# Kernel optimization log

Hardware: AMD Instinct MI355X
Metric: run time of the kernel (lower is better)

Reference implementation:

```python
import jax, jax.numpy as jnp
import numpy as np
from jax import lax

IN_DIM, MID_DIM, OUT_DIM, SIZE_EMBED_DIM = 1024, 512, 50, 64
N_POS = 30
B, N = 4, 512
H = MID_DIM // 2  # per-direction LSTM hidden


def _span_size_ids(n):
    ar = jnp.arange(n)
    ids = ar[None, :] - ar[:, None]          # [i,j] = j - i
    ids = jnp.where(ids < -(N_POS // 2), -(N_POS // 2), ids)
    ids = jnp.where(ids >= N_POS // 2, N_POS // 2 - 1, ids) + N_POS // 2
    return ids.astype(jnp.int32)             # values in [0, 29]


def _lstm_dir(x, Wih, Whh, bih, bhh, reverse):
    # x: (B, N, in_dim) -> (B, N, H)
    b = x.shape[0]
    xs = jnp.swapaxes(x, 0, 1)               # (N, B, in)
    init = (jnp.zeros((b, H), x.dtype), jnp.zeros((b, H), x.dtype))

    def step(carry, xt):
        h, c = carry
        g = xt @ Wih.T + h @ Whh.T + (bih + bhh)
        i, f, gg, o = jnp.split(g, 4, axis=-1)
        c = jax.nn.sigmoid(f) * c + jax.nn.sigmoid(i) * jnp.tanh(gg)
        h = jax.nn.sigmoid(o) * jnp.tanh(c)
        return (h, c), h

    _, hs = lax.scan(step, init, xs, reverse=reverse)
    return jnp.swapaxes(hs, 0, 1)


def setup_inputs() -> dict:
    key = jax.random.key(0)
    ks = jax.random.split(key, 16)
    s = 0.02
    d = {
        'input_embeds': jax.random.normal(ks[0], (B, N, IN_DIM), jnp.float32),
        'Wih_f': jax.random.normal(ks[1], (4 * H, IN_DIM)) * s,
        'Whh_f': jax.random.normal(ks[2], (4 * H, H)) * s,
        'bih_f': jnp.zeros((4 * H,)),
        'bhh_f': jnp.zeros((4 * H,)),
        'Wih_b': jax.random.normal(ks[3], (4 * H, IN_DIM)) * s,
        'Whh_b': jax.random.normal(ks[4], (4 * H, H)) * s,
        'bih_b': jnp.zeros((4 * H,)),
        'bhh_b': jnp.zeros((4 * H,)),
        'W_head': jax.random.normal(ks[5], (MID_DIM, MID_DIM)) * s,
        'b_head': jnp.zeros((MID_DIM,)),
        'W_tail': jax.random.normal(ks[6], (MID_DIM, MID_DIM)) * s,
        'b_tail': jnp.zeros((MID_DIM,)),
        'emb_table': jax.random.normal(ks[7], (N_POS, SIZE_EMBED_DIM)) * s,
        'W': jax.random.normal(ks[8], (OUT_DIM, 2 * MID_DIM + SIZE_EMBED_DIM + 2)) * s,
    }
    return d


def reference(input_embeds, Wih_f, Whh_f, bih_f, bhh_f, Wih_b, Whh_b, bih_b, bhh_b,
              W_head, b_head, W_tail, b_tail, emb_table, W):
    n = input_embeds.shape[1]
    # BiLSTM (dropouts are identity at eval)
    h_f = _lstm_dir(input_embeds, Wih_f, Whh_f, bih_f, bhh_f, reverse=False)
    h_b = _lstm_dir(input_embeds, Wih_b, Whh_b, bih_b, bhh_b, reverse=True)
    x = jnp.concatenate([h_f, h_b], axis=-1)              # (B, N, mid)
    head = jax.nn.leaky_relu(x @ W_head.T + b_head)        # (B, N, mid)
    tail = jax.nn.leaky_relu(x @ W_tail.T + b_tail)
    ones = jnp.ones_like(head[..., :1])
    head1 = jnp.concatenate([head, ones], axis=-1)         # (B, N, mid+1)
    tail1 = jnp.concatenate([tail, ones], axis=-1)
    se = emb_table[_span_size_ids(n)]                      # (N, N, se)
    # einsum('bmnh,kh->bkmn', cat([head1_m, tail1_n, se_mn]), W) decomposed:
    mp1 = MID_DIM + 1
    Wh, Wt, Ws = W[:, :mp1], W[:, mp1:2 * mp1], W[:, 2 * mp1:]
    s_head = jnp.einsum('bmh,kh->bkm', head1, Wh)          # (B, k, N)
    s_tail = jnp.einsum('bnh,kh->bkn', tail1, Wt)
    s_size = jnp.einsum('mnh,kh->kmn', se, Ws)             # (k, N, N)
    return s_head[:, :, :, None] + s_tail[:, :, None, :] + s_size[None]
```

## Files before the change

kernel.cpp:

```cpp
#include <hip/hip_runtime.h>
#include <hip/hip_bf16.h>
#include <stdint.h>


typedef float  floatx4 __attribute__((ext_vector_type(4)));
typedef short  short4v __attribute__((ext_vector_type(4)));
typedef short  short8  __attribute__((ext_vector_type(8)));
typedef int    int4v   __attribute__((ext_vector_type(4)));

#define LOG2E_F  1.4426950408889634f
#define TWOLOG2E_F 2.8853900817779268f

__device__ __forceinline__ short f2bf(float f) {
    __hip_bfloat16 h = __float2bfloat16(f);
    return *reinterpret_cast<short*>(&h);
}
__device__ __forceinline__ float fexp2(float x) {
#if __has_builtin(__builtin_amdgcn_exp2f)
    return __builtin_amdgcn_exp2f(x);
#else
    float r; asm("v_exp_f32 %0, %1" : "=v"(r) : "v"(x)); return r;
#endif
}
__device__ __forceinline__ float frcp(float x) {
#if __has_builtin(__builtin_amdgcn_rcpf)
    return __builtin_amdgcn_rcpf(x);
#else
    float r; asm("v_rcp_f32 %0, %1" : "=v"(r) : "v"(x)); return r;
#endif
}
__device__ __forceinline__ int q8i(float x) {
    int q = (int)rintf(x);
    return q > 127 ? 127 : (q < -127 ? -127 : q);
}

__global__ __launch_bounds__(256) void prep_k(
    const float* __restrict__ input_embeds,
    const float* __restrict__ Wih_f, const float* __restrict__ Wih_b,
    const float* __restrict__ W_head, const float* __restrict__ W_tail,
    const float* __restrict__ W, const float* __restrict__ emb,
    const float* __restrict__ bih_f, const float* __restrict__ bhh_f,
    const float* __restrict__ bih_b, const float* __restrict__ bhh_b,
    const float* __restrict__ b_head, const float* __restrict__ b_tail,
    float* __restrict__ ssize, float* __restrict__ sbias,
    float* __restrict__ biasc1, float* __restrict__ biasc2,
    __hip_bfloat16* __restrict__ abf, __hip_bfloat16* __restrict__ wihbf,
    __hip_bfloat16* __restrict__ wc2bf, __hip_bfloat16* __restrict__ wcbf)
{
    const int g0 = blockIdx.x * 256 + threadIdx.x;
    const int gs = gridDim.x * 256;

    for (int i4 = g0; i4 < (2048 * 1024) / 4; i4 += gs) {
        floatx4 v = *(const floatx4*)(input_embeds + (size_t)i4 * 4);
        short4v s = { f2bf(v[0]), f2bf(v[1]), f2bf(v[2]), f2bf(v[3]) };
        *(short4v*)(abf + (size_t)i4 * 4) = s;
    }
    for (int i4 = g0; i4 < (2048 * 1024) / 4; i4 += gs) {
        int r = i4 >> 8, c4 = (i4 & 255) * 4;
        const float* src = (r < 1024) ? (Wih_f + (size_t)r * 1024 + c4)
                                      : (Wih_b + (size_t)(r - 1024) * 1024 + c4);
        floatx4 v = *(const floatx4*)src;
        short4v s = { f2bf(v[0]), f2bf(v[1]), f2bf(v[2]), f2bf(v[3]) };
        *(short4v*)(wihbf + (size_t)i4 * 4) = s;
    }
    for (int i4 = g0; i4 < (1024 * 512) / 4; i4 += gs) {
        int r = i4 >> 7, c4 = (i4 & 127) * 4;
        const float* src = (r < 512) ? (W_head + (size_t)r * 512 + c4)
                                     : (W_tail + (size_t)(r - 512) * 512 + c4);
        floatx4 v = *(const floatx4*)src;
        short4v s = { f2bf(v[0]), f2bf(v[1]), f2bf(v[2]), f2bf(v[3]) };
        *(short4v*)(wc2bf + (size_t)i4 * 4) = s;
    }
    for (int i4 = g0; i4 < (128 * 512) / 4; i4 += gs) {
        int r = i4 >> 7, c4 = (i4 & 127) * 4;
        short4v s = {0, 0, 0, 0};
        if (r < 50) {
            const float* p = W + (size_t)r * 1090 + c4;
            s[0] = f2bf(p[0]); s[1] = f2bf(p[1]); s[2] = f2bf(p[2]); s[3] = f2bf(p[3]);
        } else if (r >= 64 && r < 114) {
            const float* p = W + (size_t)(r - 64) * 1090 + 513 + c4;
            s[0] = f2bf(p[0]); s[1] = f2bf(p[1]); s[2] = f2bf(p[2]); s[3] = f2bf(p[3]);
        }
        *(short4v*)(wcbf + (size_t)i4 * 4) = s;
    }

    for (int i = g0; i < 1600; i += gs) {
        int k = i >> 5, pp = i & 31;
        float acc = 0.0f;
        if (pp < 30)
            for (int h = 0; h < 64; ++h)
                acc += W[(size_t)k * 1090 + 1026 + h] * emb[pp * 64 + h];
        ssize[i] = acc;
    }
    for (int i = g0; i < 128; i += gs) {
        float v = 0.0f;
        if (i < 50)                    v = W[(size_t)i * 1090 + 512];
        else if (i >= 64 && i < 114)   v = W[(size_t)(i - 64) * 1090 + 1025];
        sbias[i] = v;
    }
    for (int i = g0; i < 2048; i += gs)
        biasc1[i] = (i < 1024) ? (bih_f[i] + bhh_f[i]) : (bih_b[i - 1024] + bhh_b[i - 1024]);
    for (int i = g0; i < 1024; i += gs)
        biasc2[i] = (i < 512) ? b_head[i] : b_tail[i - 512];
}

__global__ __launch_bounds__(256) void gemm_bt(
    const __hip_bfloat16* __restrict__ Abf, int lda,
    int a_split_n, int a_split_off,
    const __hip_bfloat16* __restrict__ Bbf, int ldb,
    const float* __restrict__ bias, int K, int mode,
    float* __restrict__ out0, __hip_bfloat16* __restrict__ out1)
{
    __shared__ __align__(16) short As[128][48];
    __shared__ __align__(16) short Bs[64][48];
    const int tid   = threadIdx.x;
    const int nbase = blockIdx.x * 64;
    const int mbase = blockIdx.y * 128;
    const int aoff  = (nbase >= a_split_n) ? a_split_off : 0;
    const int arow = tid >> 1, akq = (tid & 1) * 16;
    const int brow = tid >> 2, bkq = (tid & 3) * 8;
    const int wv = tid >> 6, ln = tid & 63, l15 = ln & 15, quad = ln >> 4;

    floatx4 acc[2][4];
#pragma unroll
    for (int i = 0; i < 2; ++i)
#pragma unroll
        for (int j = 0; j < 4; ++j) acc[i][j] = (floatx4){0.f, 0.f, 0.f, 0.f};

    const unsigned short* A = (const unsigned short*)Abf;
    const unsigned short* B = (const unsigned short*)Bbf;
    const int KI = K >> 5;
    for (int kk = 0; kk < KI; ++kk) {
        const unsigned short* pa = A + (size_t)(mbase + arow) * lda + aoff + kk * 32 + akq;
        short8 sa0 = *(const short8*)pa;
        short8 sa1 = *(const short8*)(pa + 8);
        const unsigned short* pb = B + (size_t)(nbase + brow) * ldb + kk * 32 + bkq;
        short8 sb = *(const short8*)pb;

        __syncthreads();
        *(short8*)&As[arow][akq]     = sa0;
        *(short8*)&As[arow][akq + 8] = sa1;
        *(short8*)&Bs[brow][bkq]     = sb;
        __syncthreads();

        short8 a0 = *(const short8*)&As[wv * 32 + l15][quad * 8];
        short8 a1 = *(const short8*)&As[wv * 32 + 16 + l15][quad * 8];
#pragma unroll
        for (int nt = 0; nt < 4; ++nt) {
            short8 bb = *(const short8*)&Bs[nt * 16 + l15][quad * 8];
            acc[0][nt] = __builtin_amdgcn_mfma_f32_16x16x32_bf16(a0, bb, acc[0][nt], 0, 0, 0);
            acc[1][nt] = __builtin_amdgcn_mfma_f32_16x16x32_bf16(a1, bb, acc[1][nt], 0, 0, 0);
        }
    }

#pragma unroll
    for (int mt = 0; mt < 2; ++mt)
#pragma unroll
        for (int nt = 0; nt < 4; ++nt) {
            const int gc = nbase + nt * 16 + l15;
            const float bv = bias[gc];
#pragma unroll
            for (int r = 0; r < 4; ++r) {
                const int gr = mbase + wv * 32 + mt * 16 + quad * 4 + r;
                float v = acc[mt][nt][r] + bv;
                if (mode == 0) {
                    const int d = gc >> 10, nn = gc & 1023;
                    const int gate = nn >> 8;
                    const int vrow = ((nn & 255) << 2) | gate;
                    const int t = gr & 511, b = gr >> 9;
                    const float gsc = (gate == 2) ? TWOLOG2E_F : -LOG2E_F;
                    out0[(((size_t)d * 512 + t) * 4 + b) * 1024 + vrow] = v * gsc;
                } else if (mode == 1) {
                    v = v < 0.0f ? 0.01f * v : v;
                    out1[(size_t)gr * 1024 + gc] = __float2bfloat16(v);
                } else {
                    out0[(size_t)gr * 128 + gc] = v;
                }
            }
        }
}

__global__ __launch_bounds__(1024) void lstm_k(
    const float* __restrict__ Whh_f, const float* __restrict__ Whh_b,
    const float* __restrict__ xg, __hip_bfloat16* __restrict__ hcat)
{
    const int dir = blockIdx.x;
    const float* Whh = dir ? Whh_b : Whh_f;
    const float* xgd = xg + (size_t)dir * 512 * 4 * 1024;
    __shared__ __align__(16) float sm_lds[1024];
    __shared__ __align__(16) signed char hq[2][4][64][16];
    __shared__ __align__(16) int gexch[16][64][4];
    const int tid = threadIdx.x;
    const int wv = tid >> 6, ln = tid & 63, l15 = ln & 15, quad = ln >> 4;

    for (int v = wv * 64; v < wv * 64 + 64; ++v) {
        const int orig = ((v & 3) << 8) | (v >> 2);
        floatx4 x = *(const floatx4*)(Whh + (size_t)orig * 256 + ln * 4);
        float m = fmaxf(fmaxf(fabsf(x[0]), fabsf(x[1])), fmaxf(fabsf(x[2]), fabsf(x[3])));
#pragma unroll
        for (int off = 32; off; off >>= 1) m = fmaxf(m, __shfl_xor(m, off, 64));
        if (ln == 0) sm_lds[v] = m;
    }
    for (int i = tid; i < 2 * 4 * 64 * 16 / 4; i += 1024) ((int*)hq)[i] = 0;
    __syncthreads();

    int4v afrag[4][4];
#pragma unroll
    for (int tt = 0; tt < 4; ++tt) {
        const int vrow = (wv * 4 + tt) * 16 + l15;
        const int orig = ((vrow & 3) << 8) | (vrow >> 2);
        const float sm = sm_lds[vrow];
        const float inv = sm > 1e-30f ? 127.0f / sm : 0.0f;
#pragma unroll
        for (int kf = 0; kf < 4; ++kf) {
            const float* p = Whh + (size_t)orig * 256 + kf * 64 + quad * 16;
            int4v fr;
#pragma unroll
            for (int j = 0; j < 4; ++j) {
                floatx4 w4 = *(const floatx4*)(p + j * 4);
                int b0 = q8i(w4[0] * inv), b1 = q8i(w4[1] * inv);
                int b2 = q8i(w4[2] * inv), b3 = q8i(w4[3] * inv);
                fr[j] = (b0 & 255) | ((b1 & 255) << 8) | ((b2 & 255) << 16) | (b3 << 24);
            }
            afrag[tt][kf] = fr;
        }
    }

    const int u_mine = wv * 16 + (ln >> 2);
    const int batch  = ln & 3;
    floatx4 scl;
    {
        const float sc = 1.0f / 16129.0f;
        floatx4 s4 = *(const floatx4*)&sm_lds[u_mine * 4];
        scl[0] = s4[0] * (sc * -LOG2E_F);
        scl[1] = s4[1] * (sc * -LOG2E_F);
        scl[2] = s4[2] * (sc *  TWOLOG2E_F);
        scl[3] = s4[3] * (sc * -LOG2E_F);
    }
    signed char* hq_w = &hq[0][u_mine >> 6][(((u_mine >> 4) & 3) << 4) + batch][u_mine & 15];
    const int t0 = dir ? 511 : 0;
    const ptrdiff_t xstep = dir ? -4096 : 4096;
    const ptrdiff_t hstep = dir ? -512 : 512;
    const float* xp = xgd + (size_t)batch * 1024 + u_mine * 4 + (size_t)t0 * 4096;
    __hip_bfloat16* hc_p = hcat + (size_t)batch * 512 * 512 + dir * 256 + u_mine
                                + (size_t)t0 * 512;

    float c = 0.0f;
    const int4v z4 = {0, 0, 0, 0};
    __syncthreads();

    floatx4 xga = *(const floatx4*)xp;
    floatx4 xgb;

#define LSTM_STEP(P, XC, XN)                                                    \
    {                                                                           \
        xp += xstep;                                                            \
        XN = *(const floatx4*)xp;   \
        int4v bb0 = *(const int4v*)&hq[P][0][ln][0];                            \
        int4v bb1 = *(const int4v*)&hq[P][1][ln][0];                            \
        int4v bb2 = *(const int4v*)&hq[P][2][ln][0];                            \
        int4v bb3 = *(const int4v*)&hq[P][3][ln][0];                            \
        int4v acc[4];                                                           \
        _Pragma("unroll")                                                       \
        for (int tt = 0; tt < 4; ++tt) {                                        \
            int4v t0v = __builtin_amdgcn_mfma_i32_16x16x64_i8(                  \
                afrag[tt][0], bb0, z4, 0, 0, 0);                                \
            t0v = __builtin_amdgcn_mfma_i32_16x16x64_i8(                        \
                afrag[tt][1], bb1, t0v, 0, 0, 0);                               \
            t0v = __builtin_amdgcn_mfma_i32_16x16x64_i8(                        \
                afrag[tt][2], bb2, t0v, 0, 0, 0);                               \
            acc[tt] = __builtin_amdgcn_mfma_i32_16x16x64_i8(                    \
                afrag[tt][3], bb3, t0v, 0, 0, 0);                               \
        }                                                                       \
        if (l15 < 4) {                                                          \
            _Pragma("unroll")                                                   \
            for (int tt = 0; tt < 4; ++tt)                                      \
                *(int4v*)&gexch[wv][(tt * 4 + quad) * 4 + l15][0] = acc[tt];    \
        }                                                                       \
        int4v g = *(const int4v*)&gexch[wv][ln][0];                             \
        float gi = fmaf((float)g[0], scl[0], XC[0]);                            \
        float gf = fmaf((float)g[1], scl[1], XC[1]);                            \
        float gg = fmaf((float)g[2], scl[2], XC[2]);                            \
        float go = fmaf((float)g[3], scl[3], XC[3]);                            \
        float iv = frcp(1.0f + fexp2(gi));           \
        float fv = frcp(1.0f + fexp2(gf));                                      \
        float tg = fmaf(-2.0f, frcp(1.0f + fexp2(gg)), 1.0f);         \
        float ov = frcp(1.0f + fexp2(go));                                      \
        c = fmaf(fv, c, iv * tg);                                               \
        float tc = fmaf(-2.0f, frcp(1.0f + fexp2(c * TWOLOG2E_F)), 1.0f);       \
        float h = ov * tc;                                                      \
        *hc_p = __float2bfloat16(h);                                            \
        hq_w[(P) ? 0 : 4096] = (signed char)(int)rintf(h * 127.0f);  \
        hc_p += hstep;                                                          \
        asm volatile("s_waitcnt lgkmcnt(0)" ::: "memory");                      \
        __builtin_amdgcn_s_barrier();                                           \
        __builtin_amdgcn_sched_barrier(0);                                      \
        asm volatile("" ::: "memory");                                          \
    }

    for (int s = 0; s < 512; s += 2) {
        LSTM_STEP(0, xga, xgb)
        LSTM_STEP(1, xgb, xga)
    }
#undef LSTM_STEP
}

__global__ __launch_bounds__(256) void final_k(
    const float* __restrict__ sarr, const float* __restrict__ ssize,
    float* __restrict__ out)
{
    const int mb = blockIdx.x * 64;
    const int k  = blockIdx.y;
    const int b  = blockIdx.z;
    __shared__ float st[512];
    __shared__ float sh[64];
    __shared__ float ss[32];
    const int tid = threadIdx.x;
    for (int n = tid; n < 512; n += 256)
        st[n] = sarr[((size_t)b * 512 + n) * 128 + 64 + k];
    if (tid < 64) sh[tid] = sarr[((size_t)b * 512 + mb + tid) * 128 + k];
    if (tid < 32) ss[tid] = ssize[k * 32 + tid];
    __syncthreads();
    const int n4 = (tid & 127) * 4;
    const int m0 = tid >> 7;
    float* ob = out + (((size_t)b * 50 + k) * 512 + mb) * 512;
    for (int mi = m0; mi < 64; mi += 2) {
        const int m = mb + mi;
        const float base = sh[mi];
        floatx4 v;
#pragma unroll
        for (int e = 0; e < 4; ++e) {
            int d = n4 + e - m;
            d = d < -15 ? -15 : (d > 14 ? 14 : d);
            v[e] = base + st[n4 + e] + ss[d + 15];
        }
        *(floatx4*)(ob + (size_t)mi * 512 + n4) = v;
    }
}

extern "C" void kernel_launch(void* const* d_in, const int* in_sizes, int n_in,
                              void* d_out, int out_size, void* d_ws, size_t ws_size,
                              hipStream_t stream)
{
    const float* input_embeds = (const float*)d_in[0];
    const float* Wih_f  = (const float*)d_in[1];
    const float* Whh_f  = (const float*)d_in[2];
    const float* bih_f  = (const float*)d_in[3];
    const float* bhh_f  = (const float*)d_in[4];
    const float* Wih_b  = (const float*)d_in[5];
    const float* Whh_b  = (const float*)d_in[6];
    const float* bih_b  = (const float*)d_in[7];
    const float* bhh_b  = (const float*)d_in[8];
    const float* W_head = (const float*)d_in[9];
    const float* b_head = (const float*)d_in[10];
    const float* W_tail = (const float*)d_in[11];
    const float* b_tail = (const float*)d_in[12];
    const float* emb    = (const float*)d_in[13];
    const float* W      = (const float*)d_in[14];
    float* out = (float*)d_out;

    char* w = (char*)d_ws;
    float* xg     = (float*)w;  w += (size_t)2 * 512 * 4 * 1024 * 4;
    float* biasc1 = (float*)w;  w += 2048 * 4;
    float* biasc2 = (float*)w;  w += 1024 * 4;
    float* sbias  = (float*)w;  w += 128 * 4;
    float* ssize  = (float*)w;  w += 1600 * 4;
    __hip_bfloat16* wcbf  = (__hip_bfloat16*)w;  w += (size_t)128 * 512 * 2;
    __hip_bfloat16* wihbf = (__hip_bfloat16*)w;  w += (size_t)2048 * 1024 * 2;
    __hip_bfloat16* hcat  = (__hip_bfloat16*)w;  w += (size_t)2048 * 512 * 2;
    float* sarr = (float*)w;
    __hip_bfloat16* wc2bf = (__hip_bfloat16*)w;  w += (size_t)1024 * 512 * 2;
    __hip_bfloat16* abf   = (__hip_bfloat16*)w;
    __hip_bfloat16* ht    = (__hip_bfloat16*)w;  w += (size_t)2048 * 1024 * 2;

    hipLaunchKernelGGL(prep_k, dim3(64), dim3(256), 0, stream,
        input_embeds, Wih_f, Wih_b, W_head, W_tail, W, emb,
        bih_f, bhh_f, bih_b, bhh_b, b_head, b_tail,
        ssize, sbias, biasc1, biasc2, abf, wihbf, wc2bf, wcbf);

    hipLaunchKernelGGL(gemm_bt, dim3(32, 16), dim3(256), 0, stream,
        abf, 1024, 1 << 30, 0,
        wihbf, 1024, biasc1, 1024, 0, xg, (__hip_bfloat16*)nullptr);

    hipLaunchKernelGGL(lstm_k, dim3(2), dim3(1024), 0, stream, Whh_f, Whh_b, xg, hcat);

    hipLaunchKernelGGL(gemm_bt, dim3(16, 16), dim3(256), 0, stream,
        hcat, 512, 1 << 30, 0,
        wc2bf, 512, biasc2, 512, 1, (float*)nullptr, ht);

    hipLaunchKernelGGL(gemm_bt, dim3(2, 16), dim3(256), 0, stream,
        ht, 1024, 64, 512,
        wcbf, 512, sbias, 512, 2, sarr, (__hip_bfloat16*)nullptr);

    hipLaunchKernelGGL(final_k, dim3(8, 50, 4), dim3(256), 0, stream, sarr, ssize, out);
}
```

Baseline: 859.9 us.

## Compact LSTM h buffer, reorder gate layout, transpose score array, nontemporal output stores

Several layout changes land together. The input-gate GEMM now writes the gate projections gate-major, and each LSTM thread gathers its four gates with strided scalar loads. The quantized hidden-state LDS buffer is shrunk to only the batch columns that are actually used, with lanes outside them feeding zero B-fragments. The head/tail score array is stored transposed so the final kernel reads it contiguously, and the final kernel's large output is written with nontemporal stores to avoid polluting the cache. The risk is that four scalar loads per step replace one vector load on the serial recurrence path.

```diff
diff --git a/kernel.cpp b/kernel.cpp
--- a/kernel.cpp
+++ b/kernel.cpp
@@ -165,16 +165,15 @@
                 float v = acc[mt][nt][r] + bv;
                 if (mode == 0) {
                     const int d = gc >> 10, nn = gc & 1023;
-                    const int gate = nn >> 8;
-                    const int vrow = ((nn & 255) << 2) | gate;
+                    const int g = nn >> 8, u = nn & 255;
                     const int t = gr & 511, b = gr >> 9;
-                    const float gsc = (gate == 2) ? TWOLOG2E_F : -LOG2E_F;
-                    out0[(((size_t)d * 512 + t) * 4 + b) * 1024 + vrow] = v * gsc;
+                    const float gsc = (g == 2) ? TWOLOG2E_F : -LOG2E_F;
+                    out0[((((size_t)d * 512 + t) * 4 + b) * 4 + g) * 256 + u] = v * gsc;
                 } else if (mode == 1) {
                     v = v < 0.0f ? 0.01f * v : v;
                     out1[(size_t)gr * 1024 + gc] = __float2bfloat16(v);
                 } else {
-                    out0[(size_t)gr * 128 + gc] = v;
+                    out0[(size_t)gc * 2048 + gr] = v;
                 }
             }
         }
@@ -188,7 +187,7 @@
     const float* Whh = dir ? Whh_b : Whh_f;
     const float* xgd = xg + (size_t)dir * 512 * 4 * 1024;
     __shared__ __align__(16) float sm_lds[1024];
-    __shared__ __align__(16) signed char hq[2][4][64][16];
+    __shared__ __align__(16) signed char hq[2][4][16][16];
     __shared__ __align__(16) int gexch[16][64][4];
     const int tid = threadIdx.x;
     const int wv = tid >> 6, ln = tid & 63, l15 = ln & 15, quad = ln >> 4;
@@ -201,7 +200,7 @@
         for (int off = 32; off; off >>= 1) m = fmaxf(m, __shfl_xor(m, off, 64));
         if (ln == 0) sm_lds[v] = m;
     }
-    for (int i = tid; i < 2 * 4 * 64 * 16 / 4; i += 1024) ((int*)hq)[i] = 0;
+    for (int i = tid; i < 2 * 4 * 16 * 16 / 4; i += 1024) ((int*)hq)[i] = 0;
     __syncthreads();
 
     int4v afrag[4][4];
@@ -237,11 +236,12 @@
         scl[2] = s4[2] * (sc *  TWOLOG2E_F);
         scl[3] = s4[3] * (sc * -LOG2E_F);
     }
-    signed char* hq_w = &hq[0][u_mine >> 6][(((u_mine >> 4) & 3) << 4) + batch][u_mine & 15];
+    signed char* hq_w = &hq[0][u_mine >> 6][(((u_mine >> 4) & 3) << 2) + batch][u_mine & 15];
+    const int bslot = (ln >> 4) * 4 + l15;
     const int t0 = dir ? 511 : 0;
     const ptrdiff_t xstep = dir ? -4096 : 4096;
     const ptrdiff_t hstep = dir ? -512 : 512;
-    const float* xp = xgd + (size_t)batch * 1024 + u_mine * 4 + (size_t)t0 * 4096;
+    const float* xp = xgd + (size_t)batch * 1024 + u_mine + (size_t)t0 * 4096;
     __hip_bfloat16* hc_p = hcat + (size_t)batch * 512 * 512 + dir * 256 + u_mine
                                 + (size_t)t0 * 512;
 
@@ -249,17 +249,20 @@
     const int4v z4 = {0, 0, 0, 0};
     __syncthreads();
 
-    floatx4 xga = *(const floatx4*)xp;
-    floatx4 xgb;
+    floatx4 xga, xgb;
+    xga[0] = xp[0]; xga[1] = xp[256]; xga[2] = xp[512]; xga[3] = xp[768];
 
 #define LSTM_STEP(P, XC, XN)                                                    \
     {                                                                           \
         xp += xstep;                                                            \
-        XN = *(const floatx4*)xp;   \
-        int4v bb0 = *(const int4v*)&hq[P][0][ln][0];                            \
-        int4v bb1 = *(const int4v*)&hq[P][1][ln][0];                            \
-        int4v bb2 = *(const int4v*)&hq[P][2][ln][0];                            \
-        int4v bb3 = *(const int4v*)&hq[P][3][ln][0];                            \
+        XN[0] = xp[0]; XN[1] = xp[256]; XN[2] = xp[512]; XN[3] = xp[768];       \
+        int4v bb0 = z4, bb1 = z4, bb2 = z4, bb3 = z4;                           \
+        if (l15 < 4) {                                                          \
+            bb0 = *(const int4v*)&hq[P][0][bslot][0];                           \
+            bb1 = *(const int4v*)&hq[P][1][bslot][0];                           \
+            bb2 = *(const int4v*)&hq[P][2][bslot][0];                           \
+            bb3 = *(const int4v*)&hq[P][3][bslot][0];                           \
+        }                                                                       \
         int4v acc[4];                                                           \
         _Pragma("unroll")                                                       \
         for (int tt = 0; tt < 4; ++tt) {                                        \
@@ -290,7 +293,7 @@
         float tc = fmaf(-2.0f, frcp(1.0f + fexp2(c * TWOLOG2E_F)), 1.0f);       \
         float h = ov * tc;                                                      \
         *hc_p = __float2bfloat16(h);                                            \
-        hq_w[(P) ? 0 : 4096] = (signed char)(int)rintf(h * 127.0f);  \
+        hq_w[(P) ? 0 : 1024] = (signed char)(int)rintf(h * 127.0f);  \
         hc_p += hstep;                                                          \
         asm volatile("s_waitcnt lgkmcnt(0)" ::: "memory");                      \
         __builtin_amdgcn_s_barrier();                                           \
@@ -306,7 +309,7 @@
 }
 
 __global__ __launch_bounds__(256) void final_k(
-    const float* __restrict__ sarr, const float* __restrict__ ssize,
+    const float* __restrict__ sarrT, const float* __restrict__ ssize,
     float* __restrict__ out)
 {
     const int mb = blockIdx.x * 64;
@@ -317,8 +320,8 @@
     __shared__ float ss[32];
     const int tid = threadIdx.x;
     for (int n = tid; n < 512; n += 256)
-        st[n] = sarr[((size_t)b * 512 + n) * 128 + 64 + k];
-    if (tid < 64) sh[tid] = sarr[((size_t)b * 512 + mb + tid) * 128 + k];
+        st[n] = sarrT[(size_t)(64 + k) * 2048 + b * 512 + n];
+    if (tid < 64) sh[tid] = sarrT[(size_t)k * 2048 + b * 512 + mb + tid];
     if (tid < 32) ss[tid] = ssize[k * 32 + tid];
     __syncthreads();
     const int n4 = (tid & 127) * 4;
@@ -334,7 +337,7 @@
             d = d < -15 ? -15 : (d > 14 ? 14 : d);
             v[e] = base + st[n4 + e] + ss[d + 15];
         }
-        *(floatx4*)(ob + (size_t)mi * 512 + n4) = v;
+        __builtin_nontemporal_store(v, (floatx4*)(ob + (size_t)mi * 512 + n4));
     }
 }
 
@@ -368,7 +371,7 @@
     __hip_bfloat16* wcbf  = (__hip_bfloat16*)w;  w += (size_t)128 * 512 * 2;
     __hip_bfloat16* wihbf = (__hip_bfloat16*)w;  w += (size_t)2048 * 1024 * 2;
     __hip_bfloat16* hcat  = (__hip_bfloat16*)w;  w += (size_t)2048 * 512 * 2;
-    float* sarr = (float*)w;
+    float* sarrT = (float*)w;
     __hip_bfloat16* wc2bf = (__hip_bfloat16*)w;  w += (size_t)1024 * 512 * 2;
     __hip_bfloat16* abf   = (__hip_bfloat16*)w;
     __hip_bfloat16* ht    = (__hip_bfloat16*)w;  w += (size_t)2048 * 1024 * 2;
@@ -390,7 +393,7 @@
 
     hipLaunchKernelGGL(gemm_bt, dim3(2, 16), dim3(256), 0, stream,
         ht, 1024, 64, 512,
-        wcbf, 512, sbias, 512, 2, sarr, (__hip_bfloat16*)nullptr);
-
-    hipLaunchKernelGGL(final_k, dim3(8, 50, 4), dim3(256), 0, stream, sarr, ssize, out);
-}
+        wcbf, 512, sbias, 512, 2, sarrT, (__hip_bfloat16*)nullptr);
+
+    hipLaunchKernelGGL(final_k, dim3(8, 50, 4), dim3(256), 0, stream, sarrT, ssize, out);
+}
```

Result: slower. 948.1 us (+10.3%).
